# Kernel tuning notes

Measured on AMD Instinct MI355X. Metric: run time of the kernel, lower is better.

Reference implementation:

```python
import jax, jax.numpy as jnp
import numpy as np

N = 32768; D = 384; P = 3; CORR_D = 2 * 49 * P * P  # 882
G_KK = 4096; G_JK = 512
EPS = 1e-3  # LayerNorm eps in the torch module

FLOAT_NAMES = ("net","inp","corr","corr_w1","corr_b1","corr_w2","corr_b2","corr_ln_g","corr_ln_b","corr_w3","corr_b3","norm_g","norm_b","c1_w1","c1_b1","c1_w2","c1_b2","c2_w1","c2_b1","c2_w2","c2_b2","kk_fw","kk_fb","kk_gw","kk_gb","kk_hw","kk_hb","ij_fw","ij_fb","ij_gw","ij_gb","ij_hw","ij_hb","g_ln1_g","g_ln1_b","g1_gw","g1_gb","g1_r1w","g1_r1b","g1_r2w","g1_r2b","g_ln2_g","g_ln2_b","g2_gw","g2_gb","g2_r1w","g2_r1b","g2_r2w","g2_r2b","d_w","d_b","w_w","w_b")

def _ln(x, g, b):
    m = jnp.mean(x, -1, keepdims=True)
    v = jnp.mean((x - m) ** 2, -1, keepdims=True)
    return (x - m) * jax.lax.rsqrt(v + EPS) * g + b

def _mlp2(x, w1, b1, w2, b2):
    return jax.nn.relu(x @ w1 + b1) @ w2 + b2

def _gated_residual(x, gw, gb, r1w, r1b, r2w, r2b):
    gate = jax.nn.sigmoid(x @ gw + gb)
    res = jax.nn.relu(x @ r1w + r1b) @ r2w + r2b
    return x + gate * res

def _soft_agg(x, jx, fw, fb, gw, gb, hw, hb, num_groups):
    # x: [N, D]; jx: [N] group ids -> group-wise softmax weighted sum
    logits = x @ gw + gb
    feats = x @ fw + fb
    gmax = jax.ops.segment_max(logits, jx, num_segments=num_groups)
    e = jnp.exp(logits - gmax[jx])
    den = jax.ops.segment_sum(e, jx, num_segments=num_groups)
    w = e / (den[jx] + 1e-12)
    y = jax.ops.segment_sum(feats * w, jx, num_segments=num_groups)
    return (y @ hw + hb)[jx]

def _forward(p, nix, njx, ukk, ujk):
    # corr encoder MLP
    h = jax.nn.relu(p["corr"] @ p["corr_w1"] + p["corr_b1"]) @ p["corr_w2"] + p["corr_b2"]
    h = jax.nn.relu(_ln(h, p["corr_ln_g"], p["corr_ln_b"])) @ p["corr_w3"] + p["corr_b3"]
    net = p["net"] + p["inp"] + h
    net = _ln(net, p["norm_g"], p["norm_b"])
    mask_ix = (nix >= 0).astype(net.dtype).reshape(1, -1, 1)
    mask_jx = (njx >= 0).astype(net.dtype).reshape(1, -1, 1)
    net = net + _mlp2(mask_ix * net[:, nix], p["c1_w1"], p["c1_b1"], p["c1_w2"], p["c1_b2"])
    net = net + _mlp2(mask_jx * net[:, njx], p["c2_w1"], p["c2_b1"], p["c2_w2"], p["c2_b2"])
    net = net + _soft_agg(net[0], ukk, p["kk_fw"], p["kk_fb"], p["kk_gw"], p["kk_gb"], p["kk_hw"], p["kk_hb"], G_KK)[None]
    net = net + _soft_agg(net[0], ujk, p["ij_fw"], p["ij_fb"], p["ij_gw"], p["ij_gb"], p["ij_hw"], p["ij_hb"], G_JK)[None]
    net = _ln(net, p["g_ln1_g"], p["g_ln1_b"])
    net = _gated_residual(net, p["g1_gw"], p["g1_gb"], p["g1_r1w"], p["g1_r1b"], p["g1_r2w"], p["g1_r2b"])
    net = _ln(net, p["g_ln2_g"], p["g_ln2_b"])
    net = _gated_residual(net, p["g2_gw"], p["g2_gb"], p["g2_r1w"], p["g2_r1b"], p["g2_r2w"], p["g2_r2b"])
    r = jax.nn.relu(net)
    d = r @ p["d_w"] + p["d_b"]               # GradClip is identity in forward
    w = jax.nn.sigmoid(r @ p["w_w"] + p["w_b"])
    return net, d, w

def setup_inputs() -> dict:
    key = jax.random.key(0)
    it = iter(jax.random.split(key, 64))
    def pr(*shape):
        return jax.random.normal(next(it), shape, dtype=jnp.float32) * 0.02
    z = lambda *s: jnp.zeros(s, jnp.float32)
    o = lambda *s: jnp.ones(s, jnp.float32)
    inp = {
        "net": jax.random.normal(next(it), (1, N, D), dtype=jnp.float32),
        "inp": jax.random.normal(next(it), (1, N, D), dtype=jnp.float32),
        "corr": jax.random.normal(next(it), (1, N, CORR_D), dtype=jnp.float32),
        "nix": jax.random.randint(next(it), (N,), 0, N),
        "njx": jax.random.randint(next(it), (N,), 0, N),
        "ukk": jax.random.randint(next(it), (N,), 0, G_KK),
        "ujk": jax.random.randint(next(it), (N,), 0, G_JK),
        "corr_w1": pr(CORR_D, D), "corr_b1": z(D), "corr_w2": pr(D, D), "corr_b2": z(D),
        "corr_ln_g": o(D), "corr_ln_b": z(D), "corr_w3": pr(D, D), "corr_b3": z(D),
        "norm_g": o(D), "norm_b": z(D),
        "c1_w1": pr(D, D), "c1_b1": z(D), "c1_w2": pr(D, D), "c1_b2": z(D),
        "c2_w1": pr(D, D), "c2_b1": z(D), "c2_w2": pr(D, D), "c2_b2": z(D),
        "kk_fw": pr(D, D), "kk_fb": z(D), "kk_gw": pr(D, D), "kk_gb": z(D), "kk_hw": pr(D, D), "kk_hb": z(D),
        "ij_fw": pr(D, D), "ij_fb": z(D), "ij_gw": pr(D, D), "ij_gb": z(D), "ij_hw": pr(D, D), "ij_hb": z(D),
        "g_ln1_g": o(D), "g_ln1_b": z(D),
        "g1_gw": pr(D, D), "g1_gb": z(D), "g1_r1w": pr(D, D), "g1_r1b": z(D), "g1_r2w": pr(D, D), "g1_r2b": z(D),
        "g_ln2_g": o(D), "g_ln2_b": z(D),
        "g2_gw": pr(D, D), "g2_gb": z(D), "g2_r1w": pr(D, D), "g2_r1b": z(D), "g2_r2w": pr(D, D), "g2_r2b": z(D),
        "d_w": pr(D, 2), "d_b": z(2), "w_w": pr(D, 2), "w_b": z(2),
    }
    return inp

def reference(net, inp, corr, corr_w1, corr_b1, corr_w2, corr_b2, corr_ln_g, corr_ln_b, corr_w3, corr_b3, norm_g, norm_b, c1_w1, c1_b1, c1_w2, c1_b2, c2_w1, c2_b1, c2_w2, c2_b2, kk_fw, kk_fb, kk_gw, kk_gb, kk_hw, kk_hb, ij_fw, ij_fb, ij_gw, ij_gb, ij_hw, ij_hb, g_ln1_g, g_ln1_b, g1_gw, g1_gb, g1_r1w, g1_r1b, g1_r2w, g1_r2b, g_ln2_g, g_ln2_b, g2_gw, g2_gb, g2_r1w, g2_r1b, g2_r2w, g2_r2b, d_w, d_b, w_w, w_b, nix, njx, ukk, ujk):
    loc = locals()
    fl = {k: loc[k] for k in FLOAT_NAMES}
    return _forward(fl, nix, njx, ukk, ujk)
```

## Files before the change

### kernel.cpp

```cpp
#include <hip/hip_runtime.h>
#include <hip/hip_bf16.h>
#include <math.h>

#define NR 32768
#define DD 384
#define CDM 882
#define CDMP 896

typedef float f4 __attribute__((ext_vector_type(4)));
typedef float f32x4 __attribute__((ext_vector_type(4)));
typedef __bf16 bf16x8 __attribute__((ext_vector_type(8)));
typedef __bf16 bf16x4 __attribute__((ext_vector_type(4)));

__device__ inline f4 ld4(const float* p) { f4 v; __builtin_memcpy(&v, p, 16); return v; }
__device__ inline void st4(float* p, f4 v) { __builtin_memcpy(p, &v, 16); }
__device__ inline bf16x8 ld8h(const __bf16* p) { bf16x8 v; __builtin_memcpy(&v, p, 16); return v; }
__device__ inline void st8h(__bf16* p, bf16x8 v) { __builtin_memcpy(p, &v, 16); }

__device__ inline void gl_lds16(const void* g, void* l) {
  __builtin_amdgcn_global_load_lds(
      (const __attribute__((address_space(1))) void*)g,
      (__attribute__((address_space(3))) void*)l, 16, 0, 0);
}

__device__ inline float gred16(float v) {
#pragma unroll
  for (int o = 1; o < 16; o <<= 1) v += __shfl_xor(v, o, 64);
  return v;
}

__global__ __launch_bounds__(256) void corr2bf16_k(const float* __restrict__ src,
                                                   __bf16* __restrict__ dst) {
  int i = blockIdx.x * 256 + threadIdx.x;
  int row = i / 112, c8 = (i - row * 112) * 8;
  const float* sp = src + (size_t)row * CDM + c8;
  bf16x8 h;
  if (c8 + 8 <= CDM) {
#pragma unroll
    for (int e = 0; e < 8; ++e) h[e] = (__bf16)sp[e];
  } else {
#pragma unroll
    for (int e = 0; e < 8; ++e) h[e] = (c8 + e < CDM) ? (__bf16)sp[e] : (__bf16)0.f;
  }
  st8h(dst + (size_t)row * CDMP + c8, h);
}

struct WPtrs { const float* w[18]; };

__global__ __launch_bounds__(256) void trans_all_k(WPtrs P, __bf16* __restrict__ dst) {
  int wi = blockIdx.y;
  const float* W = P.w[wi];
  __bf16* WT = dst + (size_t)wi * DD * DD;
  int i = blockIdx.x * 256 + threadIdx.x;
  if (i >= DD * DD) return;
  int n = i / DD, k = i - n * DD;
  WT[i] = (__bf16)W[(size_t)k * DD + n];
}

__global__ __launch_bounds__(256) void trans_corr_k(const float* __restrict__ W,
                                                    __bf16* __restrict__ WT) {
  int i = blockIdx.x * 256 + threadIdx.x;
  if (i >= DD * CDMP) return;
  int n = i / CDMP, k = i - n * CDMP;
  WT[i] = (k < CDM) ? (__bf16)W[(size_t)k * DD + n] : (__bf16)0.f;
}

template <int EPI, int AFP32>
__global__ __launch_bounds__(256, 2) void gemm_k(
    const void* __restrict__ Av, const __bf16* __restrict__ WT,
    const float* __restrict__ bias, __bf16* __restrict__ OUT,
    const __bf16* __restrict__ XRES, const int* __restrict__ idx,
    const __bf16* __restrict__ zpage, int M, int K, int Kreal, int nwg) {
  __shared__ __align__(16) __bf16 sm[2][128 * 64];
  const int t = threadIdx.x;
  const int w = t >> 6, lane = t & 63;
  int orig = blockIdx.x;
  int q = nwg >> 3, r = nwg & 7, xcd = orig & 7, lid = orig >> 3;
  int wg = (xcd < r ? xcd * (q + 1) : r * (q + 1) + (xcd - r) * q) + lid;
  const int m0 = (wg / 3) * 128;
  const int n0 = (wg % 3) * 128;
  const int fr = lane & 15, fq = lane >> 4;
  const int wr = (w >> 1) * 64, wc = (w & 1) * 64;

  const __bf16* bptr[4];
  const __bf16* aptr[4];
  int aadv[4];
#pragma unroll
  for (int j = 0; j < 4; ++j) {
    int rloc = w * 32 + j * 8 + (lane >> 3);
    int cch = (lane & 7) ^ (rloc & 7);
    bptr[j] = WT + (size_t)(n0 + rloc) * K + cch * 8;
    if constexpr (!AFP32) {
      int gm = m0 + rloc;
      int ar = idx ? idx[gm] : gm;
      if (ar >= 0) { aptr[j] = (const __bf16*)Av + (size_t)ar * K + cch * 8; aadv[j] = 64; }
      else { aptr[j] = zpage; aadv[j] = 0; }
    }
  }
  const float* Af = (const float*)Av;
  const int NT = K >> 6;

  f32x4 acc[4][4];
#pragma unroll
  for (int a = 0; a < 4; ++a)
#pragma unroll
    for (int b = 0; b < 4; ++b)
#pragma unroll
      for (int j = 0; j < 4; ++j) acc[a][b][j] = 0.f;

  auto stage = [&](int k0) {
    __bf16* As = sm[0];
    __bf16* Bs = sm[1];
    if constexpr (AFP32) {
#pragma unroll
      for (int p = 0; p < 4; ++p) {
        int rr = p * 32 + (t >> 3);
        int cc = t & 7;
        int kb = k0 + cc * 8;
        const float* ap = Af + (size_t)(m0 + rr) * Kreal + kb;
        float vv[8];
        if (kb + 8 <= Kreal) {
          f4 v0 = ld4(ap), v1 = ld4(ap + 4);
#pragma unroll
          for (int e = 0; e < 4; ++e) { vv[e] = v0[e]; vv[4 + e] = v1[e]; }
        } else {
#pragma unroll
          for (int e = 0; e < 8; ++e) vv[e] = (kb + e < Kreal) ? ap[e] : 0.f;
        }
        bf16x8 h;
#pragma unroll
        for (int e = 0; e < 8; ++e) h[e] = (__bf16)vv[e];
        *reinterpret_cast<bf16x8*>(&As[rr * 64 + (((cc ^ (rr & 7)) << 3))]) = h;
      }
    } else {
#pragma unroll
      for (int j = 0; j < 4; ++j) {
        gl_lds16(aptr[j], &As[(w * 32 + j * 8) * 64]);
        aptr[j] += aadv[j];
      }
    }
#pragma unroll
    for (int j = 0; j < 4; ++j) {
      gl_lds16(bptr[j], &Bs[(w * 32 + j * 8) * 64]);
      bptr[j] += 64;
    }
  };

  auto compute = [&]() {
    const __bf16* As = sm[0];
    const __bf16* Bs = sm[1];
#pragma unroll
    for (int kk2 = 0; kk2 < 2; ++kk2) {
      bf16x8 af[4], bv[4];
#pragma unroll
      for (int mi = 0; mi < 4; ++mi) {
        int rr = wr + mi * 16 + fr;
        af[mi] = *reinterpret_cast<const bf16x8*>(
            &As[rr * 64 + (((fq + kk2 * 4) ^ (rr & 7)) << 3)]);
      }
#pragma unroll
      for (int ni = 0; ni < 4; ++ni) {
        int rr = wc + ni * 16 + fr;
        bv[ni] = *reinterpret_cast<const bf16x8*>(
            &Bs[rr * 64 + (((fq + kk2 * 4) ^ (rr & 7)) << 3)]);
      }
#pragma unroll
      for (int mi = 0; mi < 4; ++mi)
#pragma unroll
        for (int ni = 0; ni < 4; ++ni)
          acc[mi][ni] = __builtin_amdgcn_mfma_f32_16x16x32_bf16(af[mi], bv[ni],
                                                                acc[mi][ni], 0, 0, 0);
    }
  };

  for (int tt = 0; tt < NT; ++tt) {
    if (tt) __syncthreads();
    stage(tt << 6);
    __syncthreads();
    compute();
  }

#pragma unroll
  for (int mi = 0; mi < 4; ++mi)
#pragma unroll
    for (int ni = 0; ni < 4; ++ni) {
      int col = n0 + wc + ni * 16 + fr;
      float bvv = bias[col];
#pragma unroll
      for (int j = 0; j < 4; ++j) {
        int row = m0 + wr + mi * 16 + fq * 4 + j;
        size_t o = (size_t)row * DD + col;
        float v = acc[mi][ni][j] + bvv;
        if constexpr (EPI == 0) {
          OUT[o] = (__bf16)v;
        } else if constexpr (EPI == 1) {
          OUT[o] = (__bf16)fmaxf(v, 0.f);
        } else if constexpr (EPI == 2) {
          OUT[o] = (__bf16)((float)OUT[o] + v);
        } else {
          float gl = (float)OUT[o];
          float g = 1.f / (1.f + expf(-gl));
          OUT[o] = (__bf16)((float)XRES[o] + g * v);
        }
      }
    }
}

template <int RELU>
__global__ __launch_bounds__(256) void ln_k(const __bf16* __restrict__ x,
                                            const float* __restrict__ g,
                                            const float* __restrict__ b,
                                            __bf16* __restrict__ out) {
  int w = threadIdx.x >> 6, lane = threadIdx.x & 63;
  int s = lane & 15, qq = lane >> 4;
  int row = blockIdx.x * 16 + w * 4 + qq;
  size_t base = (size_t)row * DD;
  float v[24];
#pragma unroll
  for (int i = 0; i < 3; ++i) {
    bf16x8 h = ld8h(x + base + (s + 16 * i) * 8);
#pragma unroll
    for (int e = 0; e < 8; ++e) v[i * 8 + e] = (float)h[e];
  }
  float sm = 0.f;
#pragma unroll
  for (int i = 0; i < 24; ++i) sm += v[i];
  sm = gred16(sm);
  float mean = sm * (1.f / 384.f);
  float qs = 0.f;
#pragma unroll
  for (int i = 0; i < 24; ++i) { float d = v[i] - mean; qs += d * d; }
  qs = gred16(qs);
  float rs = rsqrtf(qs * (1.f / 384.f) + 1e-3f);
#pragma unroll
  for (int i = 0; i < 3; ++i) {
    int col = (s + 16 * i) * 8;
    f4 g0 = ld4(g + col), g1 = ld4(g + col + 4);
    f4 b0 = ld4(b + col), b1 = ld4(b + col + 4);
    bf16x8 o;
#pragma unroll
    for (int e = 0; e < 4; ++e) {
      float y0 = (v[i * 8 + e] - mean) * rs * g0[e] + b0[e];
      float y1 = (v[i * 8 + 4 + e] - mean) * rs * g1[e] + b1[e];
      if (RELU) { y0 = fmaxf(y0, 0.f); y1 = fmaxf(y1, 0.f); }
      o[e] = (__bf16)y0; o[4 + e] = (__bf16)y1;
    }
    st8h(out + base + col, o);
  }
}

__global__ __launch_bounds__(256) void ln3_k(const float* __restrict__ x1,
                                             const float* __restrict__ x2,
                                             const __bf16* __restrict__ x3,
                                             const float* __restrict__ g,
                                             const float* __restrict__ b,
                                             __bf16* __restrict__ out) {
  int w = threadIdx.x >> 6, lane = threadIdx.x & 63;
  int s = lane & 15, qq = lane >> 4;
  int row = blockIdx.x * 16 + w * 4 + qq;
  size_t base = (size_t)row * DD;
  float v[24];
#pragma unroll
  for (int i = 0; i < 3; ++i) {
    int col = (s + 16 * i) * 8;
    f4 a0 = ld4(x1 + base + col), a1 = ld4(x1 + base + col + 4);
    f4 c0 = ld4(x2 + base + col), c1 = ld4(x2 + base + col + 4);
    bf16x8 h = ld8h(x3 + base + col);
#pragma unroll
    for (int e = 0; e < 4; ++e) {
      v[i * 8 + e] = a0[e] + c0[e] + (float)h[e];
      v[i * 8 + 4 + e] = a1[e] + c1[e] + (float)h[4 + e];
    }
  }
  float sm = 0.f;
#pragma unroll
  for (int i = 0; i < 24; ++i) sm += v[i];
  sm = gred16(sm);
  float mean = sm * (1.f / 384.f);
  float qs = 0.f;
#pragma unroll
  for (int i = 0; i < 24; ++i) { float d = v[i] - mean; qs += d * d; }
  qs = gred16(qs);
  float rs = rsqrtf(qs * (1.f / 384.f) + 1e-3f);
#pragma unroll
  for (int i = 0; i < 3; ++i) {
    int col = (s + 16 * i) * 8;
    f4 g0 = ld4(g + col), g1 = ld4(g + col + 4);
    f4 b0 = ld4(b + col), b1 = ld4(b + col + 4);
    bf16x8 o;
#pragma unroll
    for (int e = 0; e < 4; ++e) {
      o[e] = (__bf16)((v[i * 8 + e] - mean) * rs * g0[e] + b0[e]);
      o[4 + e] = (__bf16)((v[i * 8 + 4 + e] - mean) * rs * g1[e] + b1[e]);
    }
    st8h(out + base + col, o);
  }
}

__global__ __launch_bounds__(256) void hist_k(const int* __restrict__ gid,
                                              int* __restrict__ cnt, int n) {
  int i = blockIdx.x * 256 + threadIdx.x;
  if (i < n) atomicAdd(&cnt[gid[i]], 1);
}

__global__ __launch_bounds__(256) void scan_k(const int* __restrict__ cnt,
                                              int* __restrict__ off, int G) {
  __shared__ int ls[256];
  int t = threadIdx.x;
  int per = G / 256;
  int base = t * per;
  int s = 0;
  for (int i = 0; i < per; ++i) s += cnt[base + i];
  ls[t] = s;
  __syncthreads();
  for (int o = 1; o < 256; o <<= 1) {
    int v = (t >= o) ? ls[t - o] : 0;
    __syncthreads();
    ls[t] += v;
    __syncthreads();
  }
  int run = (t == 0) ? 0 : ls[t - 1];
  for (int i = 0; i < per; ++i) {
    off[base + i] = run;
    run += cnt[base + i];
  }
  if (t == 255) off[G] = run;
}

__global__ __launch_bounds__(256) void scatter_k(const int* __restrict__ gid,
                                                 const int* __restrict__ off,
                                                 int* __restrict__ cur,
                                                 int* __restrict__ rows, int n) {
  int i = blockIdx.x * 256 + threadIdx.x;
  if (i >= n) return;
  int g = gid[i];
  int p = atomicAdd(&cur[g], 1);
  rows[off[g] + p] = i;
}

__global__ __launch_bounds__(384) void segagg_k(const __bf16* __restrict__ L,
                                                const __bf16* __restrict__ Ft,
                                                const int* __restrict__ rows,
                                                const int* __restrict__ off,
                                                float* __restrict__ yb) {
  int g = blockIdx.x;
  int c = threadIdx.x;
  int s = off[g], e = off[g + 1];
  float mx = -3.0e38f;
  for (int p = s; p < e; ++p) {
    int r = rows[p];
    mx = fmaxf(mx, (float)L[(size_t)r * DD + c]);
  }
  float num = 0.f, den = 0.f;
  for (int p = s; p < e; ++p) {
    int r = rows[p];
    float lv = (float)L[(size_t)r * DD + c];
    float fv = (float)Ft[(size_t)r * DD + c];
    float ev = expf(lv - mx);
    den += ev;
    num += fv * ev;
  }
  yb[(size_t)g * DD + c] = num / (den + 1e-12f);
}

__global__ __launch_bounds__(256) void addgather_k(__bf16* __restrict__ X,
                                                   const __bf16* __restrict__ z,
                                                   const int* __restrict__ gid) {
  int i = blockIdx.x * 256 + threadIdx.x;
  int row = i / 48, c = (i - row * 48) * 8;
  int g = gid[row];
  size_t lo = (size_t)row * DD + c;
  bf16x8 a = ld8h(X + lo);
  bf16x8 zz = ld8h(z + (size_t)g * DD + c);
  bf16x8 o;
#pragma unroll
  for (int e = 0; e < 8; ++e) o[e] = (__bf16)((float)a[e] + (float)zz[e]);
  st8h(X + lo, o);
}

__global__ __launch_bounds__(256) void final_k(const __bf16* __restrict__ net,
                                               const float* __restrict__ dw,
                                               const float* __restrict__ db,
                                               const float* __restrict__ ww,
                                               const float* __restrict__ wb,
                                               float* __restrict__ out) {
  int w = threadIdx.x >> 6, lane = threadIdx.x & 63;
  int s = lane & 15, qq = lane >> 4;
  int row = blockIdx.x * 16 + w * 4 + qq;
  size_t base = (size_t)row * DD;
  float d0 = 0, d1 = 0, w0 = 0, w1 = 0;
#pragma unroll
  for (int i = 0; i < 3; ++i) {
    int col = (s + 16 * i) * 8;
    bf16x8 h = ld8h(net + base + col);
    f4 o0, o1;
#pragma unroll
    for (int e = 0; e < 4; ++e) {
      float x0 = (float)h[e], x1 = (float)h[4 + e];
      o0[e] = x0; o1[e] = x1;
      float r0 = fmaxf(x0, 0.f), r1 = fmaxf(x1, 0.f);
      int c0 = col + e, c1 = col + 4 + e;
      d0 += r0 * dw[2 * c0] + r1 * dw[2 * c1];
      d1 += r0 * dw[2 * c0 + 1] + r1 * dw[2 * c1 + 1];
      w0 += r0 * ww[2 * c0] + r1 * ww[2 * c1];
      w1 += r0 * ww[2 * c0 + 1] + r1 * ww[2 * c1 + 1];
    }
    st4(out + base + col, o0);
    st4(out + base + col + 4, o1);
  }
  d0 = gred16(d0); d1 = gred16(d1); w0 = gred16(w0); w1 = gred16(w1);
  if (s == 0) {
    float* outd = out + (size_t)NR * DD;
    float* outw = outd + (size_t)NR * 2;
    outd[2 * row] = d0 + db[0];
    outd[2 * row + 1] = d1 + db[1];
    outw[2 * row] = 1.f / (1.f + expf(-(w0 + wb[0])));
    outw[2 * row + 1] = 1.f / (1.f + expf(-(w1 + wb[1])));
  }
}

extern "C" void kernel_launch(void* const* d_in, const int* in_sizes, int n_in,
                              void* d_out, int out_size, void* d_ws, size_t ws_size,
                              hipStream_t stream) {
  const float* in_net = (const float*)d_in[0];
  const float* in_inp = (const float*)d_in[1];
  const float* in_corr = (const float*)d_in[2];
  const int* nix = (const int*)d_in[3];
  const int* njx = (const int*)d_in[4];
  const int* ukk = (const int*)d_in[5];
  const int* ujk = (const int*)d_in[6];
  auto F = [&](int i) { return (const float*)d_in[i]; };

  constexpr size_t MiB = 1024 * 1024;
  constexpr size_t SZ_ACT = (size_t)NR * DD * 2;
  char* ws = (char*)d_ws;
  __bf16* Xc = (__bf16*)(ws);
  __bf16* T2b = (__bf16*)(ws);
  __bf16* Fb = (__bf16*)(ws + SZ_ACT);
  __bf16* zb = (__bf16*)(ws + 2 * SZ_ACT);
  float* yb = (float*)(ws + 2 * SZ_ACT + 3 * MiB);
  __bf16* T1b = (__bf16*)(ws + 60 * MiB);
  char* p = ws + 84 * MiB;
  int* rows = (int*)p; p += (size_t)NR * 4;
  int* off = (int*)p; p += 32768;
  int* cnt = (int*)p; p += 16384;
  int* curb = (int*)p; p += 16384;
  __bf16* wt_all = (__bf16*)p; p += (size_t)18 * DD * DD * 2;
  __bf16* wt_corr1 = (__bf16*)p; p += (size_t)DD * CDMP * 2;
  __bf16* zpage = (__bf16*)p;

  const int widx[18] = {17, 19, 21, 23, 25, 27, 29, 31, 33, 35, 39, 41, 43, 47, 49, 51, 9, 13};
  WPtrs P;
  for (int i = 0; i < 18; ++i) P.w[i] = F(widx[i]);
  auto WTp = [&](int i) { return wt_all + (size_t)i * DD * DD; };

  hipMemsetAsync(zpage, 0, 256, stream);
  trans_all_k<<<dim3(576, 18), 256, 0, stream>>>(P, wt_all);
  trans_corr_k<<<1344, 256, 0, stream>>>(F(7), wt_corr1);
  corr2bf16_k<<<NR * 112 / 256, 256, 0, stream>>>(in_corr, Xc);

  auto GEMM = [&](int epi, int afp32, const void* A, const __bf16* WT, const float* bias,
                  __bf16* OUT, const __bf16* XRES, const int* idx, int M, int Kp, int Kr) {
    int nwg = (M / 128) * 3;
    dim3 g(nwg), b(256);
    if (afp32) {
      gemm_k<0, 1><<<g, b, 0, stream>>>(A, WT, bias, OUT, XRES, idx, zpage, M, Kp, Kr, nwg);
    } else {
      switch (epi) {
        case 0: gemm_k<0, 0><<<g, b, 0, stream>>>(A, WT, bias, OUT, XRES, idx, zpage, M, Kp, Kr, nwg); break;
        case 1: gemm_k<1, 0><<<g, b, 0, stream>>>(A, WT, bias, OUT, XRES, idx, zpage, M, Kp, Kr, nwg); break;
        case 2: gemm_k<2, 0><<<g, b, 0, stream>>>(A, WT, bias, OUT, XRES, idx, zpage, M, Kp, Kr, nwg); break;
        default: gemm_k<3, 0><<<g, b, 0, stream>>>(A, WT, bias, OUT, XRES, idx, zpage, M, Kp, Kr, nwg); break;
      }
    }
  };

  auto SEGAGG = [&](const int* gid, int G, const __bf16* L, const __bf16* Ft) {
    hipMemsetAsync(cnt, 0, (size_t)G * 4, stream);
    hipMemsetAsync(curb, 0, (size_t)G * 4, stream);
    hist_k<<<NR / 256, 256, 0, stream>>>(gid, cnt, NR);
    scan_k<<<1, 256, 0, stream>>>(cnt, off, G);
    scatter_k<<<NR / 256, 256, 0, stream>>>(gid, off, curb, rows, NR);
    segagg_k<<<G, 384, 0, stream>>>(L, Ft, rows, off, yb);
  };

  const int LNG = NR / 16;
  const int SEGB = NR * 48 / 256;

  GEMM(1, 0, Xc, wt_corr1, F(8), T1b, nullptr, nullptr, NR, CDMP, CDMP);
  GEMM(0, 0, T1b, WTp(16), F(10), T2b, nullptr, nullptr, NR, DD, DD);
  ln_k<1><<<LNG, 256, 0, stream>>>(T2b, F(11), F(12), T1b);
  GEMM(0, 0, T1b, WTp(17), F(14), T2b, nullptr, nullptr, NR, DD, DD);
  ln3_k<<<LNG, 256, 0, stream>>>(in_net, in_inp, T2b, F(15), F(16), T1b);
  GEMM(1, 0, T1b, WTp(0), F(18), T2b, nullptr, nix, NR, DD, DD);
  GEMM(2, 0, T2b, WTp(1), F(20), T1b, nullptr, nullptr, NR, DD, DD);
  GEMM(1, 0, T1b, WTp(2), F(22), T2b, nullptr, njx, NR, DD, DD);
  GEMM(2, 0, T2b, WTp(3), F(24), T1b, nullptr, nullptr, NR, DD, DD);
  GEMM(0, 0, T1b, WTp(5), F(28), T2b, nullptr, nullptr, NR, DD, DD);
  GEMM(0, 0, T1b, WTp(4), F(26), Fb, nullptr, nullptr, NR, DD, DD);
  SEGAGG(ukk, 4096, T2b, Fb);
  GEMM(0, 1, yb, WTp(6), F(30), zb, nullptr, nullptr, 4096, DD, DD);
  addgather_k<<<SEGB, 256, 0, stream>>>(T1b, zb, ukk);
  GEMM(0, 0, T1b, WTp(8), F(34), T2b, nullptr, nullptr, NR, DD, DD);
  GEMM(0, 0, T1b, WTp(7), F(32), Fb, nullptr, nullptr, NR, DD, DD);
  SEGAGG(ujk, 512, T2b, Fb);
  GEMM(0, 1, yb, WTp(9), F(36), zb, nullptr, nullptr, 512, DD, DD);
  addgather_k<<<SEGB, 256, 0, stream>>>(T1b, zb, ujk);
  ln_k<0><<<LNG, 256, 0, stream>>>(T1b, F(37), F(38), T2b);
  GEMM(0, 0, T2b, WTp(10), F(40), Fb, nullptr, nullptr, NR, DD, DD);
  GEMM(1, 0, T2b, WTp(11), F(42), T1b, nullptr, nullptr, NR, DD, DD);
  GEMM(3, 0, T1b, WTp(12), F(44), Fb, T2b, nullptr, NR, DD, DD);
  ln_k<0><<<LNG, 256, 0, stream>>>(Fb, F(45), F(46), T1b);
  GEMM(0, 0, T1b, WTp(13), F(48), T2b, nullptr, nullptr, NR, DD, DD);
  GEMM(1, 0, T1b, WTp(14), F(50), Fb, nullptr, nullptr, NR, DD, DD);
  GEMM(3, 0, Fb, WTp(15), F(52), T2b, T1b, nullptr, NR, DD, DD);
  final_k<<<LNG, 256, 0, stream>>>(T2b, F(53), F(54), F(55), F(56), (float*)d_out);
}
```

Before: 656.4 us.

## Use full-width 128x384 GEMM tiles with double-buffered async LDS loads

```diff
diff --git a/kernel.cpp b/kernel.cpp
--- a/kernel.cpp
+++ b/kernel.cpp
@@ -66,92 +66,91 @@
 }
 
 template <int EPI, int AFP32>
-__global__ __launch_bounds__(256, 2) void gemm_k(
+__global__ __launch_bounds__(512, 1) void gemm_k(
     const void* __restrict__ Av, const __bf16* __restrict__ WT,
     const float* __restrict__ bias, __bf16* __restrict__ OUT,
     const __bf16* __restrict__ XRES, const int* __restrict__ idx,
-    const __bf16* __restrict__ zpage, int M, int K, int Kreal, int nwg) {
-  __shared__ __align__(16) __bf16 sm[2][128 * 64];
+    const __bf16* __restrict__ zpage, int M, int K) {
+  __shared__ __align__(16) __bf16 sm[2 * 32768];
   const int t = threadIdx.x;
   const int w = t >> 6, lane = t & 63;
-  int orig = blockIdx.x;
-  int q = nwg >> 3, r = nwg & 7, xcd = orig & 7, lid = orig >> 3;
-  int wg = (xcd < r ? xcd * (q + 1) : r * (q + 1) + (xcd - r) * q) + lid;
-  const int m0 = (wg / 3) * 128;
-  const int n0 = (wg % 3) * 128;
+  const int m0 = blockIdx.x * 128;
   const int fr = lane & 15, fq = lane >> 4;
-  const int wr = (w >> 1) * 64, wc = (w & 1) * 64;
-
-  const __bf16* bptr[4];
-  const __bf16* aptr[4];
-  int aadv[4];
-#pragma unroll
-  for (int j = 0; j < 4; ++j) {
-    int rloc = w * 32 + j * 8 + (lane >> 3);
+  const int wr = (w >> 2) * 64, wc = (w & 3) * 96;
+
+  const __bf16* aptr[2];
+  int aadv[2];
+  const __bf16* bptr[6];
+#pragma unroll
+  for (int j = 0; j < 2; ++j) {
+    int rloc = w * 16 + j * 8 + (lane >> 3);
     int cch = (lane & 7) ^ (rloc & 7);
-    bptr[j] = WT + (size_t)(n0 + rloc) * K + cch * 8;
     if constexpr (!AFP32) {
-      int gm = m0 + rloc;
-      int ar = idx ? idx[gm] : gm;
+      int ar = idx ? idx[m0 + rloc] : (m0 + rloc);
       if (ar >= 0) { aptr[j] = (const __bf16*)Av + (size_t)ar * K + cch * 8; aadv[j] = 64; }
       else { aptr[j] = zpage; aadv[j] = 0; }
     }
   }
+#pragma unroll
+  for (int j = 0; j < 6; ++j) {
+    int rloc = w * 48 + j * 8 + (lane >> 3);
+    int cch = (lane & 7) ^ (rloc & 7);
+    bptr[j] = WT + (size_t)rloc * K + cch * 8;
+  }
   const float* Af = (const float*)Av;
   const int NT = K >> 6;
 
-  f32x4 acc[4][4];
+  f32x4 acc[4][6];
 #pragma unroll
   for (int a = 0; a < 4; ++a)
 #pragma unroll
-    for (int b = 0; b < 4; ++b)
+    for (int b = 0; b < 6; ++b)
 #pragma unroll
       for (int j = 0; j < 4; ++j) acc[a][b][j] = 0.f;
 
-  auto stage = [&](int k0) {
-    __bf16* As = sm[0];
-    __bf16* Bs = sm[1];
-    if constexpr (AFP32) {
-#pragma unroll
-      for (int p = 0; p < 4; ++p) {
-        int rr = p * 32 + (t >> 3);
-        int cc = t & 7;
-        int kb = k0 + cc * 8;
-        const float* ap = Af + (size_t)(m0 + rr) * Kreal + kb;
-        float vv[8];
-        if (kb + 8 <= Kreal) {
-          f4 v0 = ld4(ap), v1 = ld4(ap + 4);
-#pragma unroll
-          for (int e = 0; e < 4; ++e) { vv[e] = v0[e]; vv[4 + e] = v1[e]; }
-        } else {
-#pragma unroll
-          for (int e = 0; e < 8; ++e) vv[e] = (kb + e < Kreal) ? ap[e] : 0.f;
-        }
-        bf16x8 h;
-#pragma unroll
-        for (int e = 0; e < 8; ++e) h[e] = (__bf16)vv[e];
-        *reinterpret_cast<bf16x8*>(&As[rr * 64 + (((cc ^ (rr & 7)) << 3))]) = h;
-      }
-    } else {
-#pragma unroll
-      for (int j = 0; j < 4; ++j) {
-        gl_lds16(aptr[j], &As[(w * 32 + j * 8) * 64]);
-        aptr[j] += aadv[j];
-      }
-    }
-#pragma unroll
-    for (int j = 0; j < 4; ++j) {
-      gl_lds16(bptr[j], &Bs[(w * 32 + j * 8) * 64]);
+  auto stageG = [&](int buf) {
+    __bf16* As = sm + buf * 32768;
+    __bf16* Bs = As + 8192;
+#pragma unroll
+    for (int j = 0; j < 2; ++j) {
+      gl_lds16(aptr[j], &As[(w * 16 + j * 8) * 64]);
+      aptr[j] += aadv[j];
+    }
+#pragma unroll
+    for (int j = 0; j < 6; ++j) {
+      gl_lds16(bptr[j], &Bs[(w * 48 + j * 8) * 64]);
       bptr[j] += 64;
     }
   };
 
-  auto compute = [&]() {
-    const __bf16* As = sm[0];
-    const __bf16* Bs = sm[1];
+  auto stageF = [&](int k0) {
+    __bf16* As = sm;
+    __bf16* Bs = sm + 8192;
+#pragma unroll
+    for (int j = 0; j < 2; ++j) {
+      int rr = (t >> 3) + 64 * j;
+      int cc = t & 7;
+      const float* ap = Af + (size_t)(m0 + rr) * K + k0 + cc * 8;
+      f4 v0 = ld4(ap), v1 = ld4(ap + 4);
+      bf16x8 h;
+#pragma unroll
+      for (int e = 0; e < 4; ++e) { h[e] = (__bf16)v0[e]; h[4 + e] = (__bf16)v1[e]; }
+      *reinterpret_cast<bf16x8*>(&As[rr * 64 + ((cc ^ (rr & 7)) << 3)]) = h;
+    }
+#pragma unroll
+    for (int j = 0; j < 6; ++j) {
+      gl_lds16(bptr[j], &Bs[(w * 48 + j * 8) * 64]);
+      bptr[j] += 64;
+    }
+  };
+
+  auto compute = [&](int buf) {
+    const __bf16* As = sm + buf * 32768;
+    const __bf16* Bs = As + 8192;
 #pragma unroll
     for (int kk2 = 0; kk2 < 2; ++kk2) {
-      bf16x8 af[4], bv[4];
+      bf16x8 af[4];
+      bf16x8 bv[6];
 #pragma unroll
       for (int mi = 0; mi < 4; ++mi) {
         int rr = wr + mi * 16 + fr;
@@ -159,7 +158,7 @@
             &As[rr * 64 + (((fq + kk2 * 4) ^ (rr & 7)) << 3)]);
       }
 #pragma unroll
-      for (int ni = 0; ni < 4; ++ni) {
+      for (int ni = 0; ni < 6; ++ni) {
         int rr = wc + ni * 16 + fr;
         bv[ni] = *reinterpret_cast<const bf16x8*>(
             &Bs[rr * 64 + (((fq + kk2 * 4) ^ (rr & 7)) << 3)]);
@@ -167,24 +166,43 @@
 #pragma unroll
       for (int mi = 0; mi < 4; ++mi)
 #pragma unroll
-        for (int ni = 0; ni < 4; ++ni)
+        for (int ni = 0; ni < 6; ++ni)
           acc[mi][ni] = __builtin_amdgcn_mfma_f32_16x16x32_bf16(af[mi], bv[ni],
                                                                 acc[mi][ni], 0, 0, 0);
     }
   };
 
-  for (int tt = 0; tt < NT; ++tt) {
-    if (tt) __syncthreads();
-    stage(tt << 6);
-    __syncthreads();
-    compute();
+  if constexpr (AFP32) {
+    for (int tt = 0; tt < NT; ++tt) {
+      if (tt) __syncthreads();
+      stageF(tt << 6);
+      __syncthreads();
+      compute(0);
+    }
+  } else {
+    stageG(0);
+    int buf = 0;
+    for (int tt = 0; tt < NT; ++tt) {
+      if (tt + 1 < NT) {
+        stageG(buf ^ 1);
+        asm volatile("s_waitcnt vmcnt(8)" ::: "memory");
+      } else {
+        asm volatile("s_waitcnt vmcnt(0)" ::: "memory");
+      }
+      __builtin_amdgcn_s_barrier();
+      __builtin_amdgcn_sched_barrier(0);
+      compute(buf);
+      __builtin_amdgcn_s_barrier();
+      __builtin_amdgcn_sched_barrier(0);
+      buf ^= 1;
+    }
   }
 
 #pragma unroll
   for (int mi = 0; mi < 4; ++mi)
 #pragma unroll
-    for (int ni = 0; ni < 4; ++ni) {
-      int col = n0 + wc + ni * 16 + fr;
+    for (int ni = 0; ni < 6; ++ni) {
+      int col = wc + ni * 16 + fr;
       float bvv = bias[col];
 #pragma unroll
       for (int j = 0; j < 4; ++j) {
@@ -304,7 +322,8 @@
 }
 
 __global__ __launch_bounds__(256) void scan_k(const int* __restrict__ cnt,
-                                              int* __restrict__ off, int G) {
+                                              int* __restrict__ off,
+                                              int* __restrict__ curb, int G) {
   __shared__ int ls[256];
   int t = threadIdx.x;
   int per = G / 256;
@@ -323,6 +342,7 @@
   for (int i = 0; i < per; ++i) {
     off[base + i] = run;
     run += cnt[base + i];
+    curb[base + i] = 0;
   }
   if (t == 255) off[G] = run;
 }
@@ -460,26 +480,24 @@
   corr2bf16_k<<<NR * 112 / 256, 256, 0, stream>>>(in_corr, Xc);
 
   auto GEMM = [&](int epi, int afp32, const void* A, const __bf16* WT, const float* bias,
-                  __bf16* OUT, const __bf16* XRES, const int* idx, int M, int Kp, int Kr) {
-    int nwg = (M / 128) * 3;
-    dim3 g(nwg), b(256);
+                  __bf16* OUT, const __bf16* XRES, const int* idx, int M, int K) {
+    dim3 g(M / 128), b(512);
     if (afp32) {
-      gemm_k<0, 1><<<g, b, 0, stream>>>(A, WT, bias, OUT, XRES, idx, zpage, M, Kp, Kr, nwg);
+      gemm_k<0, 1><<<g, b, 0, stream>>>(A, WT, bias, OUT, XRES, idx, zpage, M, K);
     } else {
       switch (epi) {
-        case 0: gemm_k<0, 0><<<g, b, 0, stream>>>(A, WT, bias, OUT, XRES, idx, zpage, M, Kp, Kr, nwg); break;
-        case 1: gemm_k<1, 0><<<g, b, 0, stream>>>(A, WT, bias, OUT, XRES, idx, zpage, M, Kp, Kr, nwg); break;
-        case 2: gemm_k<2, 0><<<g, b, 0, stream>>>(A, WT, bias, OUT, XRES, idx, zpage, M, Kp, Kr, nwg); break;
-        default: gemm_k<3, 0><<<g, b, 0, stream>>>(A, WT, bias, OUT, XRES, idx, zpage, M, Kp, Kr, nwg); break;
+        case 0: gemm_k<0, 0><<<g, b, 0, stream>>>(A, WT, bias, OUT, XRES, idx, zpage, M, K); break;
+        case 1: gemm_k<1, 0><<<g, b, 0, stream>>>(A, WT, bias, OUT, XRES, idx, zpage, M, K); break;
+        case 2: gemm_k<2, 0><<<g, b, 0, stream>>>(A, WT, bias, OUT, XRES, idx, zpage, M, K); break;
+        default: gemm_k<3, 0><<<g, b, 0, stream>>>(A, WT, bias, OUT, XRES, idx, zpage, M, K); break;
       }
     }
   };
 
   auto SEGAGG = [&](const int* gid, int G, const __bf16* L, const __bf16* Ft) {
     hipMemsetAsync(cnt, 0, (size_t)G * 4, stream);
-    hipMemsetAsync(curb, 0, (size_t)G * 4, stream);
     hist_k<<<NR / 256, 256, 0, stream>>>(gid, cnt, NR);
-    scan_k<<<1, 256, 0, stream>>>(cnt, off, G);
+    scan_k<<<1, 256, 0, stream>>>(cnt, off, curb, G);
     scatter_k<<<NR / 256, 256, 0, stream>>>(gid, off, curb, rows, NR);
     segagg_k<<<G, 384, 0, stream>>>(L, Ft, rows, off, yb);
   };
@@ -487,32 +505,32 @@
   const int LNG = NR / 16;
   const int SEGB = NR * 48 / 256;
 
-  GEMM(1, 0, Xc, wt_corr1, F(8), T1b, nullptr, nullptr, NR, CDMP, CDMP);
-  GEMM(0, 0, T1b, WTp(16), F(10), T2b, nullptr, nullptr, NR, DD, DD);
+  GEMM(1, 0, Xc, wt_corr1, F(8), T1b, nullptr, nullptr, NR, CDMP);
+  GEMM(0, 0, T1b, WTp(16), F(10), T2b, nullptr, nullptr, NR, DD);
   ln_k<1><<<LNG, 256, 0, stream>>>(T2b, F(11), F(12), T1b);
-  GEMM(0, 0, T1b, WTp(17), F(14), T2b, nullptr, nullptr, NR, DD, DD);
+  GEMM(0, 0, T1b, WTp(17), F(14), T2b, nullptr, nullptr, NR, DD);
   ln3_k<<<LNG, 256, 0, stream>>>(in_net, in_inp, T2b, F(15), F(16), T1b);
-  GEMM(1, 0, T1b, WTp(0), F(18), T2b, nullptr, nix, NR, DD, DD);
-  GEMM(2, 0, T2b, WTp(1), F(20), T1b, nullptr, nullptr, NR, DD, DD);
-  GEMM(1, 0, T1b, WTp(2), F(22), T2b, nullptr, njx, NR, DD, DD);
-  GEMM(2, 0, T2b, WTp(3), F(24), T1b, nullptr, nullptr, NR, DD, DD);
-  GEMM(0, 0, T1b, WTp(5), F(28), T2b, nullptr, nullptr, NR, DD, DD);
-  GEMM(0, 0, T1b, WTp(4), F(26), Fb, nullptr, nullptr, NR, DD, DD);
+  GEMM(1, 0, T1b, WTp(0), F(18), T2b, nullptr, nix, NR, DD);
+  GEMM(2, 0, T2b, WTp(1), F(20), T1b, nullptr, nullptr, NR, DD);
+  GEMM(1, 0, T1b, WTp(2), F(22), T2b, nullptr, njx, NR, DD);
+  GEMM(2, 0, T2b, WTp(3), F(24), T1b, nullptr, nullptr, NR, DD);
+  GEMM(0, 0, T1b, WTp(5), F(28), T2b, nullptr, nullptr, NR, DD);
+  GEMM(0, 0, T1b, WTp(4), F(26), Fb, nullptr, nullptr, NR, DD);
   SEGAGG(ukk, 4096, T2b, Fb);
-  GEMM(0, 1, yb, WTp(6), F(30), zb, nullptr, nullptr, 4096, DD, DD);
+  GEMM(0, 1, yb, WTp(6), F(30), zb, nullptr, nullptr, 4096, DD);
   addgather_k<<<SEGB, 256, 0, stream>>>(T1b, zb, ukk);
-  GEMM(0, 0, T1b, WTp(8), F(34), T2b, nullptr, nullptr, NR, DD, DD);
-  GEMM(0, 0, T1b, WTp(7), F(32), Fb, nullptr, nullptr, NR, DD, DD);
+  GEMM(0, 0, T1b, WTp(8), F(34), T2b, nullptr, nullptr, NR, DD);
+  GEMM(0, 0, T1b, WTp(7), F(32), Fb, nullptr, nullptr, NR, DD);
   SEGAGG(ujk, 512, T2b, Fb);
-  GEMM(0, 1, yb, WTp(9), F(36), zb, nullptr, nullptr, 512, DD, DD);
+  GEMM(0, 1, yb, WTp(9), F(36), zb, nullptr, nullptr, 512, DD);
   addgather_k<<<SEGB, 256, 0, stream>>>(T1b, zb, ujk);
   ln_k<0><<<LNG, 256, 0, stream>>>(T1b, F(37), F(38), T2b);
-  GEMM(0, 0, T2b, WTp(10), F(40), Fb, nullptr, nullptr, NR, DD, DD);
-  GEMM(1, 0, T2b, WTp(11), F(42), T1b, nullptr, nullptr, NR, DD, DD);
-  GEMM(3, 0, T1b, WTp(12), F(44), Fb, T2b, nullptr, NR, DD, DD);
+  GEMM(0, 0, T2b, WTp(10), F(40), Fb, nullptr, nullptr, NR, DD);
+  GEMM(1, 0, T2b, WTp(11), F(42), T1b, nullptr, nullptr, NR, DD);
+  GEMM(3, 0, T1b, WTp(12), F(44), Fb, T2b, nullptr, NR, DD);
   ln_k<0><<<LNG, 256, 0, stream>>>(Fb, F(45), F(46), T1b);
-  GEMM(0, 0, T1b, WTp(13), F(48), T2b, nullptr, nullptr, NR, DD, DD);
-  GEMM(1, 0, T1b, WTp(14), F(50), Fb, nullptr, nullptr, NR, DD, DD);
-  GEMM(3, 0, Fb, WTp(15), F(52), T2b, T1b, nullptr, NR, DD, DD);
+  GEMM(0, 0, T1b, WTp(13), F(48), T2b, nullptr, nullptr, NR, DD);
+  GEMM(1, 0, T1b, WTp(14), F(50), Fb, nullptr, nullptr, NR, DD);
+  GEMM(3, 0, Fb, WTp(15), F(52), T2b, T1b, nullptr, NR, DD);
   final_k<<<LNG, 256, 0, stream>>>(T2b, F(53), F(54), F(55), F(56), (float*)d_out);
 }
```

New measurement: 666.2 us. About the same (+1.5%).
